# Kernel optimization log

Hardware: AMD Instinct MI355X
Metric: run time of the kernel (lower is better)

Reference implementation:

```python
import jax, jax.numpy as jnp
import numpy as np

BN_EPS = 1e-5


def _gin_layer(x, src, dst, W, b, num_nodes):
    # GINConv with eps=0: h_i = MLP(x_i + sum_{j in N(i)} x_j)
    agg = jax.ops.segment_sum(x[src], dst, num_segments=num_nodes)  # [N, F]
    h = (x + agg) @ W + b
    return jax.nn.relu(h)


def _batchnorm(h, gamma, beta):
    # training-mode BatchNorm1d: biased batch stats over the node dim
    mean = jnp.mean(h, axis=0)
    var = jnp.mean(jnp.square(h - mean), axis=0)
    return (h - mean) * jax.lax.rsqrt(var + BN_EPS) * gamma + beta


def setup_inputs() -> dict:
    key = jax.random.key(0)
    N, E, F, H = 50000, 800000, 128, 128
    ks = jax.random.split(key, 6)
    x = jax.random.normal(ks[0], (N, F), dtype=jnp.float32)
    edge_index = jax.random.randint(ks[1], (2, E), 0, N, dtype=jnp.int64)
    W1 = jax.random.normal(ks[2], (F, H), dtype=jnp.float32) * 0.05
    b1 = jnp.zeros((H,), dtype=jnp.float32)
    W2 = jax.random.normal(ks[3], (H, H), dtype=jnp.float32) * 0.05
    b2 = jnp.zeros((H,), dtype=jnp.float32)
    g1 = jnp.ones((H,), dtype=jnp.float32)
    be1 = jnp.zeros((H,), dtype=jnp.float32)
    g2 = jnp.ones((H,), dtype=jnp.float32)
    be2 = jnp.zeros((H,), dtype=jnp.float32)
    return {"x": x, "edge_index": edge_index, "W1": W1, "b1": b1,
            "W2": W2, "b2": b2, "g1": g1, "be1": be1, "g2": g2, "be2": be2}


def reference(x, edge_index, W1, b1, W2, b2, g1, be1, g2, be2):
    N = x.shape[0]
    src, dst = edge_index[0], edge_index[1]
    h = _gin_layer(x, src, dst, W1, b1, N)
    h = _batchnorm(h, g1, be1)
    h = _gin_layer(h, src, dst, W2, b2, N)
    return _batchnorm(h, g2, be2)
```

## Files before the change

### kernel.cpp

```cpp
#include <hip/hip_runtime.h>
#include <hip/hip_fp16.h>

#define FDIM 128
#define NGRP 8

typedef _Float16 half8_t __attribute__((ext_vector_type(8)));
typedef _Float16 half4_t __attribute__((ext_vector_type(4)));
typedef float float4_t __attribute__((ext_vector_type(4)));


__global__ void prep_kernel(int* __restrict__ zbase, int zn,
                            const float* __restrict__ x, _Float16* __restrict__ xh, int n4x,
                            const float* __restrict__ W1, _Float16* __restrict__ Wf1,
                            const float* __restrict__ W2, _Float16* __restrict__ Wf2,
                            int nzb, int ncb) {
  int b = blockIdx.x, t = threadIdx.x;
  if (b < nzb) {
    int i = b * 256 + t;
    if (i < zn) zbase[i] = 0;
  } else if (b < nzb + ncb) {
    int i = (b - nzb) * 256 + t;
    if (i < n4x) {
      float4 v = ((const float4*)x)[i];
      half4_t h;
      h.x = (_Float16)v.x; h.y = (_Float16)v.y; h.z = (_Float16)v.z; h.w = (_Float16)v.w;
      ((half4_t*)xh)[i] = h;
    }
  } else {
    int gid = (b - nzb - ncb) * 256 + t;
    int which = gid >> 14;
    int tid = gid & 16383;
    const float* W = which ? W2 : W1;
    _Float16* Wf = which ? Wf2 : Wf1;
    int j = tid & 7, lane = (tid >> 3) & 63, rest = tid >> 9;
    int kb = rest & 3, ct = (rest >> 2) & 1, wave = rest >> 3;
    int quad = lane >> 4, m16 = lane & 15;
    int k = kb * 32 + quad * 8 + j;
    int n = wave * 32 + ct * 16 + m16;
    Wf[tid] = (_Float16)W[k * FDIM + n];
  }
}


__global__ void hist_part_kernel(const int* __restrict__ dst, int* __restrict__ deg,
                                 int E, int step) {
  int grp = blockIdx.x & (NGRP - 1);
  int nb = gridDim.x >> 3, bid = blockIdx.x >> 3;
  int lo = grp * step, hi = lo + step;
  int E4 = E >> 2;
  const int4* d4 = (const int4*)dst;
  for (int i = bid * blockDim.x + threadIdx.x; i < E4; i += nb * blockDim.x) {
    int4 d = d4[i];
    if (d.x >= lo && d.x < hi) atomicAdd(&deg[d.x], 1);
    if (d.y >= lo && d.y < hi) atomicAdd(&deg[d.y], 1);
    if (d.z >= lo && d.z < hi) atomicAdd(&deg[d.z], 1);
    if (d.w >= lo && d.w < hi) atomicAdd(&deg[d.w], 1);
  }
  for (int e = (E4 << 2) + bid * blockDim.x + threadIdx.x; e < E; e += nb * blockDim.x) {
    int d = dst[e];
    if (d >= lo && d < hi) atomicAdd(&deg[d], 1);
  }
}

__global__ void scan_fused_kernel(const int* __restrict__ deg,
                                  unsigned long long* __restrict__ state,
                                  int* __restrict__ row_start, int* __restrict__ fill_pos,
                                  int N) {
  __shared__ int sh[256];
  __shared__ int s_excl;
  int t = threadIdx.x, b = blockIdx.x;
  int base = b * 1024 + t * 4;
  int d0 = (base + 0 < N) ? deg[base + 0] : 0;
  int d1 = (base + 1 < N) ? deg[base + 1] : 0;
  int d2 = (base + 2 < N) ? deg[base + 2] : 0;
  int d3 = (base + 3 < N) ? deg[base + 3] : 0;
  int l1 = d0, l2 = l1 + d1, l3 = l2 + d2, tot = l3 + d3;
  sh[t] = tot; __syncthreads();
  for (int off = 1; off < 256; off <<= 1) {
    int v = (t >= off) ? sh[t - off] : 0;
    __syncthreads();
    sh[t] += v;
    __syncthreads();
  }
  if (t == 0) {
    int block_sum = sh[255];
    if (b == 0) {
      atomicExch(&state[0], (2ULL << 32) | (unsigned)block_sum);
      s_excl = 0;
    } else {
      atomicExch(&state[b], (1ULL << 32) | (unsigned)block_sum);
      int excl = 0;
      int j = b - 1;
      for (;;) {
        unsigned long long v;
        do { v = atomicAdd(&state[j], 0ULL); } while ((v >> 32) == 0ULL);
        excl += (int)(unsigned)v;
        if ((v >> 32) == 2ULL) break;
        j--;
      }
      atomicExch(&state[b], (2ULL << 32) | (unsigned)(excl + block_sum));
      s_excl = excl;
    }
  }
  __syncthreads();
  int excl = sh[t] - tot + s_excl;
  if (base + 0 < N) { row_start[base + 0] = excl;      fill_pos[base + 0] = excl; }
  if (base + 1 < N) { row_start[base + 1] = excl + l1; fill_pos[base + 1] = excl + l1; }
  if (base + 2 < N) { row_start[base + 2] = excl + l2; fill_pos[base + 2] = excl + l2; }
  if (base + 3 < N) { row_start[base + 3] = excl + l3; fill_pos[base + 3] = excl + l3; }
}

__global__ void place_part_kernel(const int* __restrict__ src, const int* __restrict__ dst,
                                  int* __restrict__ fill_pos, int* __restrict__ ssrc,
                                  int E, int step) {
  int grp = blockIdx.x & (NGRP - 1);
  int nb = gridDim.x >> 3, bid = blockIdx.x >> 3;
  int lo = grp * step, hi = lo + step;
  int E4 = E >> 2;
  const int4* d4 = (const int4*)dst;
  const int4* s4 = (const int4*)src;
  for (int i = bid * blockDim.x + threadIdx.x; i < E4; i += nb * blockDim.x) {
    int4 d = d4[i];
    bool m0 = d.x >= lo && d.x < hi, m1 = d.y >= lo && d.y < hi;
    bool m2 = d.z >= lo && d.z < hi, m3 = d.w >= lo && d.w < hi;
    if (m0 | m1 | m2 | m3) {
      int4 s = s4[i];
      if (m0) ssrc[atomicAdd(&fill_pos[d.x], 1)] = s.x;
      if (m1) ssrc[atomicAdd(&fill_pos[d.y], 1)] = s.y;
      if (m2) ssrc[atomicAdd(&fill_pos[d.z], 1)] = s.z;
      if (m3) ssrc[atomicAdd(&fill_pos[d.w], 1)] = s.w;
    }
  }
  for (int e = (E4 << 2) + bid * blockDim.x + threadIdx.x; e < E; e += nb * blockDim.x) {
    int d = dst[e];
    if (d >= lo && d < hi) ssrc[atomicAdd(&fill_pos[d], 1)] = src[e];
  }
}


__device__ inline float2 up2(unsigned u) {
  __half2 h = *(__half2*)&u;
  return __half22float2(h);
}

template <bool SCALE>
__global__ void agg_kernel(const unsigned* __restrict__ xu, const int* __restrict__ row_start,
                           const int* __restrict__ deg, const int* __restrict__ ssrc,
                           const float* __restrict__ a, unsigned* __restrict__ outu, int N) {
  int wave = (blockIdx.x * blockDim.x + threadIdx.x) >> 6;
  int lane = threadIdx.x & 63;
  if (wave >= N) return;
  float2 c0 = up2(xu[(size_t)wave * 64 + lane]);
  float2 c1 = make_float2(0.f, 0.f), c2 = c1, c3 = c1;
  int start = row_start[wave], d = deg[wave];
  int k = 0;
  for (; k + 7 < d; k += 8) {
    int s0 = ssrc[start + k + 0], s1 = ssrc[start + k + 1];
    int s2 = ssrc[start + k + 2], s3 = ssrc[start + k + 3];
    int s4 = ssrc[start + k + 4], s5 = ssrc[start + k + 5];
    int s6 = ssrc[start + k + 6], s7 = ssrc[start + k + 7];
    unsigned u0 = xu[(size_t)s0 * 64 + lane], u1 = xu[(size_t)s1 * 64 + lane];
    unsigned u2 = xu[(size_t)s2 * 64 + lane], u3 = xu[(size_t)s3 * 64 + lane];
    unsigned u4 = xu[(size_t)s4 * 64 + lane], u5 = xu[(size_t)s5 * 64 + lane];
    unsigned u6 = xu[(size_t)s6 * 64 + lane], u7 = xu[(size_t)s7 * 64 + lane];
    float2 v0 = up2(u0), v1 = up2(u1), v2 = up2(u2), v3 = up2(u3);
    float2 v4 = up2(u4), v5 = up2(u5), v6 = up2(u6), v7 = up2(u7);
    c0.x += v0.x + v4.x; c0.y += v0.y + v4.y;
    c1.x += v1.x + v5.x; c1.y += v1.y + v5.y;
    c2.x += v2.x + v6.x; c2.y += v2.y + v6.y;
    c3.x += v3.x + v7.x; c3.y += v3.y + v7.y;
  }
  for (; k + 1 < d; k += 2) {
    int s0 = ssrc[start + k], s1 = ssrc[start + k + 1];
    unsigned u0 = xu[(size_t)s0 * 64 + lane], u1 = xu[(size_t)s1 * 64 + lane];
    float2 v0 = up2(u0), v1 = up2(u1);
    c0.x += v0.x; c0.y += v0.y;
    c1.x += v1.x; c1.y += v1.y;
  }
  if (k < d) {
    float2 v = up2(xu[(size_t)ssrc[start + k] * 64 + lane]);
    c0.x += v.x; c0.y += v.y;
  }
  float2 acc;
  acc.x = (c0.x + c1.x) + (c2.x + c3.x);
  acc.y = (c0.y + c1.y) + (c2.y + c3.y);
  if (SCALE) {
    float2 av = ((const float2*)a)[lane];
    acc.x *= av.x; acc.y *= av.y;
  }
  __half2 r = __float22half2_rn(acc);
  outu[(size_t)wave * 64 + lane] = *(unsigned*)&r;
}


template <bool LAYER2>
__global__ __launch_bounds__(256) void gemm_kernel(
    const _Float16* __restrict__ in, const _Float16* __restrict__ Wf,
    const float* __restrict__ bias, const float* __restrict__ r2,
    const int* __restrict__ deg, _Float16* __restrict__ outh,
    float* __restrict__ ssum, float* __restrict__ ssq,
    const float* __restrict__ gamma, const float* __restrict__ beta,
    const float* __restrict__ W2, float* __restrict__ aout, float* __restrict__ cout,
    int* __restrict__ counter, int N) {
  int t = threadIdx.x;
  int wave = t >> 6, lane = t & 63;
  int quad = lane >> 4, m16 = lane & 15;
  int row0 = blockIdx.x * 64;

  __shared__ float sdn[64];
  __shared__ float scc[FDIM];
  __shared__ int isLast;
  if (LAYER2) {
    if (t < 64) {
      int r = row0 + t;
      sdn[t] = (r < N) ? (float)(deg[r] + 1) : 0.f;
    }
    __syncthreads();
  }

  half8_t bf[2][4];
  const half8_t* wf8 = (const half8_t*)Wf;
#pragma unroll
  for (int ct = 0; ct < 2; ct++)
#pragma unroll
    for (int kb = 0; kb < 4; kb++)
      bf[ct][kb] = wf8[(size_t)(((wave * 2 + ct) * 4 + kb) * 64 + lane)];

  float4_t acc[4][2] = {};
#pragma unroll
  for (int rt = 0; rt < 4; rt++) {
    int arow = row0 + rt * 16 + m16;
    int cr = (arow < N) ? arow : N - 1;
#pragma unroll
    for (int kb = 0; kb < 4; kb++) {
      half8_t av = *(const half8_t*)(in + (size_t)cr * FDIM + kb * 32 + quad * 8);
      acc[rt][0] = __builtin_amdgcn_mfma_f32_16x16x32_f16(av, bf[0][kb], acc[rt][0], 0, 0, 0);
      acc[rt][1] = __builtin_amdgcn_mfma_f32_16x16x32_f16(av, bf[1][kb], acc[rt][1], 0, 0, 0);
    }
  }

#pragma unroll
  for (int ct = 0; ct < 2; ct++) {
    int col = wave * 32 + ct * 16 + m16;
    float bv = bias[col];
    float rv = LAYER2 ? r2[col] : 0.f;
    float s = 0.f, q = 0.f;
#pragma unroll
    for (int rt = 0; rt < 4; rt++) {
#pragma unroll
      for (int r = 0; r < 4; r++) {
        int row = row0 + rt * 16 + quad * 4 + r;
        if (row < N) {
          float v = acc[rt][ct][r] + bv;
          if (LAYER2) v += sdn[rt * 16 + quad * 4 + r] * rv;
          v = fmaxf(v, 0.f);
          outh[(size_t)row * FDIM + col] = (_Float16)v;
          s += v; q += v * v;
        }
      }
    }
    s += __shfl_xor(s, 16); q += __shfl_xor(q, 16);
    s += __shfl_xor(s, 32); q += __shfl_xor(q, 32);
    if (quad == 0) {
      atomicAdd(&ssum[col], s);
      atomicAdd(&ssq[col], q);
    }
  }

  __syncthreads();
  if (t == 0) {
    int v = atomicAdd(counter, 1);
    isLast = (v == (int)gridDim.x - 1);
  }
  __syncthreads();
  if (!isLast) return;

  float av = 0.f;
  if (t < FDIM) {
    float sm = atomicAdd(&ssum[t], 0.f);
    float qv = atomicAdd(&ssq[t], 0.f);
    float invn = 1.f / (float)N;
    float mean = sm * invn;
    float var = qv * invn - mean * mean;
    float rs = rsqrtf(var + 1e-5f);
    av = gamma[t] * rs;
    aout[t] = av;
    float cv = beta[t] - mean * av;
    if (LAYER2) cout[t] = cv;
    else scc[t] = cv;
  }
  if (!LAYER2) {
    __syncthreads();
    if (t < FDIM) {
      float acc2 = 0.f;
      for (int k = 0; k < FDIM; k++) acc2 += scc[k] * W2[k * FDIM + t];
      cout[t] = acc2;
    }
  }
}


__global__ void apply_h_kernel(const uint2* __restrict__ h4, const float* __restrict__ a,
                               const float* __restrict__ c, float4* __restrict__ out, int n4) {
  int i = blockIdx.x * blockDim.x + threadIdx.x;
  if (i < n4) {
    uint2 u = h4[i];
    float2 v0 = up2(u.x), v1 = up2(u.y);
    int c4 = i & 31;
    float4 av = ((const float4*)a)[c4];
    float4 cv = ((const float4*)c)[c4];
    float4 o;
    o.x = av.x * v0.x + cv.x;
    o.y = av.y * v0.y + cv.y;
    o.z = av.z * v1.x + cv.z;
    o.w = av.w * v1.y + cv.w;
    out[i] = o;
  }
}


extern "C" void kernel_launch(void* const* d_in, const int* in_sizes, int n_in,
                              void* d_out, int out_size, void* d_ws, size_t ws_size,
                              hipStream_t stream) {
  const float* x   = (const float*)d_in[0];
  const int*   ei  = (const int*)d_in[1];
  const float* W1  = (const float*)d_in[2];
  const float* b1  = (const float*)d_in[3];
  const float* W2  = (const float*)d_in[4];
  const float* b2  = (const float*)d_in[5];
  const float* g1  = (const float*)d_in[6];
  const float* be1 = (const float*)d_in[7];
  const float* g2  = (const float*)d_in[8];
  const float* be2 = (const float*)d_in[9];
  float* out = (float*)d_out;

  const int N = in_sizes[0] / FDIM;
  const int E = in_sizes[1] / 2;
  const int* src = ei;
  const int* dst = ei + E;

  auto align256 = [](char*& q) { q = (char*)(((uintptr_t)q + 255) & ~(uintptr_t)255); };

  char* p = (char*)d_ws;
  int* deg = (int*)p;                    p += (size_t)N * 4;
  float* stats = (float*)p;              p += 1280 * 4;
  unsigned long long* state = (unsigned long long*)p; p += 64 * 8;
  align256(p);
  int* row_start = (int*)p;  p += (size_t)N * 4; align256(p);
  int* fill_pos = (int*)p;   p += (size_t)N * 4; align256(p);
  int* ssrc = (int*)p;       p += (size_t)E * 4; align256(p);
  _Float16* xh  = (_Float16*)p; p += (size_t)N * FDIM * 2; align256(p);
  _Float16* h1  = (_Float16*)p; p += (size_t)N * FDIM * 2; align256(p);
  _Float16* h2  = (_Float16*)p; p += (size_t)N * FDIM * 2; align256(p);
  _Float16* Wf1 = (_Float16*)p; p += FDIM * FDIM * 2;
  _Float16* Wf2 = (_Float16*)p; p += FDIM * FDIM * 2;

  float* s1 = stats + 0,   *q1 = stats + 128;
  float* s2 = stats + 256, *q2 = stats + 384;
  float* a1 = stats + 512, *r2 = stats + 640;
  float* a2 = stats + 768, *c2 = stats + 896;
  int* cnt1 = (int*)(stats + 1024);
  int* cnt2 = (int*)(stats + 1025);

  const int nchunk = (N + 1023) / 1024;
  const int ntiles = (N + 63) / 64;
  const int step = (N + NGRP - 1) / NGRP;

  const int zn = N + 1280 + 128;
  const int nzb = (zn + 255) / 256;
  const int n4x = N * 32;
  const int ncb = (n4x + 255) / 256;

  prep_kernel<<<nzb + ncb + 128, 256, 0, stream>>>((int*)deg, zn, x, xh, n4x,
                                                   W1, Wf1, W2, Wf2, nzb, ncb);
  hist_part_kernel<<<NGRP * 128, 256, 0, stream>>>(dst, deg, E, step);
  scan_fused_kernel<<<nchunk, 256, 0, stream>>>(deg, state, row_start, fill_pos, N);
  place_part_kernel<<<NGRP * 128, 256, 0, stream>>>(src, dst, fill_pos, ssrc, E, step);

  agg_kernel<false><<<(N + 3) / 4, 256, 0, stream>>>((const unsigned*)xh, row_start, deg,
                                                     ssrc, nullptr, (unsigned*)h2, N);
  gemm_kernel<false><<<ntiles, 256, 0, stream>>>(h2, Wf1, b1, nullptr, nullptr, h1,
                                                 s1, q1, g1, be1, W2, a1, r2, cnt1, N);

  agg_kernel<true><<<(N + 3) / 4, 256, 0, stream>>>((const unsigned*)h1, row_start, deg,
                                                    ssrc, a1, (unsigned*)xh, N);
  gemm_kernel<true><<<ntiles, 256, 0, stream>>>(xh, Wf2, b2, r2, deg, h2,
                                                s2, q2, g2, be2, nullptr, a2, c2, cnt2, N);

  int n4 = N * 32;
  apply_h_kernel<<<(n4 + 255) / 256, 256, 0, stream>>>((const uint2*)h2, a2, c2,
                                                       (float4*)out, n4);
}
```

Measured before the change: 312.3 us.

## Fuse final BatchNorm apply into layer-2 GEMM using a grid-wide spin barrier

The layer-2 GEMM no longer writes fp16 h2. Every block holds its accumulators, waits on a global flag that the last-arriving block sets once the BN2 scale and shift are computed, and then writes the normalized fp32 output directly. This removes the separate apply kernel, the h2 round trip through memory and one launch. It relies on all blocks being co-resident; if they are not, the kernel can deadlock, and the spin wait keeps registers live across the barrier.

```diff
diff --git a/kernel.cpp b/kernel.cpp
--- a/kernel.cpp
+++ b/kernel.cpp
@@ -197,11 +197,11 @@
 __global__ __launch_bounds__(256) void gemm_kernel(
     const _Float16* __restrict__ in, const _Float16* __restrict__ Wf,
     const float* __restrict__ bias, const float* __restrict__ r2,
-    const int* __restrict__ deg, _Float16* __restrict__ outh,
+    const int* __restrict__ deg, _Float16* __restrict__ outh, float* __restrict__ outf,
     float* __restrict__ ssum, float* __restrict__ ssq,
     const float* __restrict__ gamma, const float* __restrict__ beta,
     const float* __restrict__ W2, float* __restrict__ aout, float* __restrict__ cout,
-    int* __restrict__ counter, int N) {
+    int* __restrict__ counter, int* __restrict__ flag, int N) {
   int t = threadIdx.x;
   int wave = t >> 6, lane = t & 63;
   int quad = lane >> 4, m16 = lane & 15;
@@ -254,7 +254,7 @@
           float v = acc[rt][ct][r] + bv;
           if (LAYER2) v += sdn[rt * 16 + quad * 4 + r] * rv;
           v = fmaxf(v, 0.f);
-          outh[(size_t)row * FDIM + col] = (_Float16)v;
+          if (!LAYER2) outh[(size_t)row * FDIM + col] = (_Float16)v;
           s += v; q += v * v;
         }
       }
@@ -273,48 +273,63 @@
     isLast = (v == (int)gridDim.x - 1);
   }
   __syncthreads();
-  if (!isLast) return;
-
-  float av = 0.f;
-  if (t < FDIM) {
-    float sm = atomicAdd(&ssum[t], 0.f);
-    float qv = atomicAdd(&ssq[t], 0.f);
-    float invn = 1.f / (float)N;
-    float mean = sm * invn;
-    float var = qv * invn - mean * mean;
-    float rs = rsqrtf(var + 1e-5f);
-    av = gamma[t] * rs;
-    aout[t] = av;
-    float cv = beta[t] - mean * av;
-    if (LAYER2) cout[t] = cv;
-    else scc[t] = cv;
-  }
-  if (!LAYER2) {
+
+  if (isLast) {
+    if (t < FDIM) {
+      float sm = atomicAdd(&ssum[t], 0.f);
+      float qv = atomicAdd(&ssq[t], 0.f);
+      float invn = 1.f / (float)N;
+      float mean = sm * invn;
+      float var = qv * invn - mean * mean;
+      float rs = rsqrtf(var + 1e-5f);
+      float av = gamma[t] * rs;
+      float cv = beta[t] - mean * av;
+      if (LAYER2) {
+        atomicExch(&aout[t], av);
+        atomicExch(&cout[t], cv);
+      } else {
+        aout[t] = av;
+        scc[t] = cv;
+      }
+    }
+    if (!LAYER2) {
+      __syncthreads();
+      if (t < FDIM) {
+        float acc2 = 0.f;
+        for (int k = 0; k < FDIM; k++) acc2 += scc[k] * W2[k * FDIM + t];
+        cout[t] = acc2;
+      }
+      return;
+    }
     __syncthreads();
-    if (t < FDIM) {
-      float acc2 = 0.f;
-      for (int k = 0; k < FDIM; k++) acc2 += scc[k] * W2[k * FDIM + t];
-      cout[t] = acc2;
-    }
-  }
-}
-
-
-__global__ void apply_h_kernel(const uint2* __restrict__ h4, const float* __restrict__ a,
-                               const float* __restrict__ c, float4* __restrict__ out, int n4) {
-  int i = blockIdx.x * blockDim.x + threadIdx.x;
-  if (i < n4) {
-    uint2 u = h4[i];
-    float2 v0 = up2(u.x), v1 = up2(u.y);
-    int c4 = i & 31;
-    float4 av = ((const float4*)a)[c4];
-    float4 cv = ((const float4*)c)[c4];
-    float4 o;
-    o.x = av.x * v0.x + cv.x;
-    o.y = av.y * v0.y + cv.y;
-    o.z = av.z * v1.x + cv.z;
-    o.w = av.w * v1.y + cv.w;
-    out[i] = o;
+    if (t == 0) atomicExch(flag, 1);
+  }
+
+  if (!LAYER2) return;
+
+  if (t == 0) {
+    while (atomicAdd(flag, 0) == 0) __builtin_amdgcn_s_sleep(8);
+  }
+  __syncthreads();
+#pragma unroll
+  for (int ct = 0; ct < 2; ct++) {
+    int col = wave * 32 + ct * 16 + m16;
+    float a2c = atomicAdd(&aout[col], 0.f);
+    float c2c = atomicAdd(&cout[col], 0.f);
+    float bv = bias[col];
+    float rv = r2[col];
+#pragma unroll
+    for (int rt = 0; rt < 4; rt++) {
+#pragma unroll
+      for (int r = 0; r < 4; r++) {
+        int row = row0 + rt * 16 + quad * 4 + r;
+        if (row < N) {
+          float v = acc[rt][ct][r] + bv + sdn[rt * 16 + quad * 4 + r] * rv;
+          v = fmaxf(v, 0.f);
+          outf[(size_t)row * FDIM + col] = a2c * v + c2c;
+        }
+      }
+    }
   }
 }
 
@@ -351,7 +366,7 @@
   int* ssrc = (int*)p;       p += (size_t)E * 4; align256(p);
   _Float16* xh  = (_Float16*)p; p += (size_t)N * FDIM * 2; align256(p);
   _Float16* h1  = (_Float16*)p; p += (size_t)N * FDIM * 2; align256(p);
-  _Float16* h2  = (_Float16*)p; p += (size_t)N * FDIM * 2; align256(p);
+  _Float16* tA  = (_Float16*)p; p += (size_t)N * FDIM * 2; align256(p);
   _Float16* Wf1 = (_Float16*)p; p += FDIM * FDIM * 2;
   _Float16* Wf2 = (_Float16*)p; p += FDIM * FDIM * 2;
 
@@ -361,6 +376,7 @@
   float* a2 = stats + 768, *c2 = stats + 896;
   int* cnt1 = (int*)(stats + 1024);
   int* cnt2 = (int*)(stats + 1025);
+  int* flg2 = (int*)(stats + 1026);
 
   const int nchunk = (N + 1023) / 1024;
   const int ntiles = (N + 63) / 64;
@@ -378,16 +394,12 @@
   place_part_kernel<<<NGRP * 128, 256, 0, stream>>>(src, dst, fill_pos, ssrc, E, step);
 
   agg_kernel<false><<<(N + 3) / 4, 256, 0, stream>>>((const unsigned*)xh, row_start, deg,
-                                                     ssrc, nullptr, (unsigned*)h2, N);
-  gemm_kernel<false><<<ntiles, 256, 0, stream>>>(h2, Wf1, b1, nullptr, nullptr, h1,
-                                                 s1, q1, g1, be1, W2, a1, r2, cnt1, N);
+                                                     ssrc, nullptr, (unsigned*)tA, N);
+  gemm_kernel<false><<<ntiles, 256, 0, stream>>>(tA, Wf1, b1, nullptr, nullptr, h1, nullptr,
+                                                 s1, q1, g1, be1, W2, a1, r2, cnt1, nullptr, N);
 
   agg_kernel<true><<<(N + 3) / 4, 256, 0, stream>>>((const unsigned*)h1, row_start, deg,
-                                                    ssrc, a1, (unsigned*)xh, N);
-  gemm_kernel<true><<<ntiles, 256, 0, stream>>>(xh, Wf2, b2, r2, deg, h2,
-                                                s2, q2, g2, be2, nullptr, a2, c2, cnt2, N);
-
-  int n4 = N * 32;
-  apply_h_kernel<<<(n4 + 255) / 256, 256, 0, stream>>>((const uint2*)h2, a2, c2,
-                                                       (float4*)out, n4);
-}
+                                                    ssrc, a1, (unsigned*)tA, N);
+  gemm_kernel<true><<<ntiles, 256, 0, stream>>>(tA, Wf2, b2, r2, deg, nullptr, out,
+                                                s2, q2, g2, be2, nullptr, a2, c2, cnt2, flg2, N);
+}
```

New measurement: 634.2 us. 2.03x slower.
